# Performance work log

Hardware: AMD Instinct MI355X
Metric: run time of the kernel (lower is better)

## Reference

```python
import jax, jax.numpy as jnp
import numpy as np

N, E, IN, H, K = 50000, 800000, 64, 64, 16


def _linear_params(key, fan_in, fan_out):
    kw, kb = jax.random.split(key)
    lim = 1.0 / np.sqrt(fan_in)
    W = jax.random.uniform(kw, (fan_in, fan_out), jnp.float32, -lim, lim)
    b = jax.random.uniform(kb, (fan_out,), jnp.float32, -lim, lim)
    return W, b


def setup_inputs() -> dict:
    key = jax.random.key(0)
    ks = jax.random.split(key, 16)
    x = jax.random.normal(ks[0], (N, IN), jnp.float32)
    edge_index = jax.random.randint(ks[1], (2, E), 0, N, jnp.int64)
    edge_attr = jax.random.uniform(ks[2], (E, 1), jnp.float32)
    curr_idx = jax.random.randint(ks[3], (), 0, N, jnp.int64)
    dest_idx = jax.random.randint(ks[4], (), 0, N, jnp.int64)
    neighbor_indices = jax.random.randint(ks[5], (K,), 0, N, jnp.int64)
    # GINEConv1 params: edge lift Linear(1->IN), mlp1 Linear(IN->H), Linear(H->H)
    We1, be1 = _linear_params(ks[6], 1, IN)
    W1a, b1a = _linear_params(ks[7], IN, H)
    W1b, b1b = _linear_params(ks[8], H, H)
    # GINEConv2 params: edge lift Linear(1->H), mlp2 Linear(H->H), Linear(H->H)
    We2, be2 = _linear_params(ks[9], 1, H)
    W2a, b2a = _linear_params(ks[10], H, H)
    W2b, b2b = _linear_params(ks[11], H, H)
    # Q head: lin1 Linear(3H->H), lin2 Linear(H->1)
    Wl1, bl1 = _linear_params(ks[12], 3 * H, H)
    Wl2, bl2 = _linear_params(ks[13], H, 1)
    return dict(x=x, edge_index=edge_index, curr_idx=curr_idx, dest_idx=dest_idx,
                neighbor_indices=neighbor_indices, edge_attr=edge_attr,
                We1=We1, be1=be1, W1a=W1a, b1a=b1a, W1b=W1b, b1b=b1b,
                We2=We2, be2=be2, W2a=W2a, b2a=b2a, W2b=W2b, b2b=b2b,
                Wl1=Wl1, bl1=bl1, Wl2=Wl2, bl2=bl2)


def _gine(x, src, dst, e_emb, Wa, ba, Wb, bb):
    # message = ReLU(x_j + edge_emb); aggregate = sum over incoming edges; eps = 0
    msg = jax.nn.relu(x[src] + e_emb)                      # [E, d]
    agg = jax.ops.segment_sum(msg, dst, num_segments=x.shape[0])  # [N, d]
    h = x + agg                                            # (1+eps)*x + agg
    return jax.nn.relu(h @ Wa + ba) @ Wb + bb


def reference(x, edge_index, curr_idx, dest_idx, neighbor_indices, edge_attr,
              We1, be1, W1a, b1a, W1b, b1b,
              We2, be2, W2a, b2a, W2b, b2b,
              Wl1, bl1, Wl2, bl2):
    src, dst = edge_index[0], edge_index[1]
    h = _gine(x, src, dst, edge_attr @ We1 + be1, W1a, b1a, W1b, b1b)
    h = jax.nn.relu(h)
    h = _gine(h, src, dst, edge_attr @ We2 + be2, W2a, b2a, W2b, b2b)  # [N, H]
    curr = h[curr_idx]                 # [H]
    dest = h[dest_idx]                 # [H]
    nbr = h[neighbor_indices]          # [K, H]
    k = nbr.shape[0]
    cat = jnp.concatenate([jnp.broadcast_to(curr, (k, curr.shape[0])),
                           jnp.broadcast_to(dest, (k, dest.shape[0])),
                           nbr], axis=-1)                  # [K, 3H]
    q = jax.nn.relu(cat @ Wl1 + bl1) @ Wl2 + bl2           # [K, 1]
    return q[:, 0]
```

## Files before the change

kernel.cpp:

```cpp
#include <hip/hip_runtime.h>

#define NDIM 64
#define KNBR 16
#define NT 18
#define CAP_S1 1024
#define CAP_B1 128
#define CAP_B2 128
#define EPT 16
#define SCAN_TPB 256

#define OFF_CNT  0
#define OFF_BC2  64
#define OFF_BC1  192
#define MEMSET_BYTES (192 + CAP_S1*4)
#define OFF_S1   8192
#define OFF_B1   (OFF_S1 + CAP_S1*4)
#define OFF_B2   (OFF_B1 + CAP_S1*CAP_B1*4)
#define OFF_H    (OFF_B2 + 32*CAP_B2*4)
#define OFF_SLOT (OFF_H + CAP_S1*NDIM*4)

__device__ __forceinline__ int imin(int a, int b) { return a < b ? a : b; }

__device__ __forceinline__ void claim_node(int v, int* sm, int* cnt, int* s1list) {
    int cur = sm[v];
    while (!(cur >= 1 && cur <= CAP_S1) && cur != -2) {
        int old = atomicCAS(&sm[v], cur, -2);
        if (old == cur) {
            int s = atomicAdd(&cnt[0], 1);
            if (s < CAP_S1) s1list[s] = v;
            __threadfence();
            sm[v] = s + 1;
            return;
        }
        cur = old;
    }
}

__global__ void __launch_bounds__(SCAN_TPB)
k_scan1(const int* __restrict__ src, const int* __restrict__ dst, int E,
        const int* __restrict__ curr, const int* __restrict__ dest,
        const int* __restrict__ nbr,
        int* cnt, int* sm, int* s1list, int* bc2, int* b2) {
    int t0[NT];
    t0[0] = curr[0];
    t0[1] = dest[0];
    #pragma unroll
    for (int j = 0; j < KNBR; ++j) t0[2 + j] = nbr[j];
    if (blockIdx.x == 0 && threadIdx.x < NT)
        claim_node(t0[threadIdx.x], sm, cnt, s1list);

    const int i4base = blockIdx.x * (SCAN_TPB * EPT / 4);
    const int nI4 = E >> 2;
    int dv[EPT];
    #pragma unroll
    for (int q = 0; q < EPT / 4; ++q) {
        int idx = i4base + q * SCAN_TPB + threadIdx.x;
        if (idx < nI4) {
            int4 v = ((const int4*)dst)[idx];
            dv[q*4+0] = v.x; dv[q*4+1] = v.y; dv[q*4+2] = v.z; dv[q*4+3] = v.w;
        } else {
            #pragma unroll
            for (int j = 0; j < 4; ++j) {
                int e = idx * 4 + j;
                dv[q*4+j] = (e < E) ? dst[e] : -1;
            }
        }
    }
    #pragma unroll
    for (int q = 0; q < EPT; ++q) {
        int dd = dv[q];
        if (dd < 0) continue;
        int e = (i4base + (q >> 2) * SCAN_TPB + threadIdx.x) * 4 + (q & 3);
        bool any = false;
        #pragma unroll
        for (int k = 0; k < NT; ++k) {
            if (dd == t0[k]) {
                any = true;
                int idx = atomicAdd(&bc2[k], 1);
                if (idx < CAP_B2) b2[k * CAP_B2 + idx] = e;
            }
        }
        if (any) claim_node(src[e], sm, cnt, s1list);
    }
}

__global__ void __launch_bounds__(SCAN_TPB)
k_scan2(const int* __restrict__ dst, int E, const int* __restrict__ sm,
        int* bc1, int* b1) {
    const int i4base = blockIdx.x * (SCAN_TPB * EPT / 4);
    const int nI4 = E >> 2;
    int dv[EPT];
    #pragma unroll
    for (int q = 0; q < EPT / 4; ++q) {
        int idx = i4base + q * SCAN_TPB + threadIdx.x;
        if (idx < nI4) {
            int4 v = ((const int4*)dst)[idx];
            dv[q*4+0] = v.x; dv[q*4+1] = v.y; dv[q*4+2] = v.z; dv[q*4+3] = v.w;
        } else {
            #pragma unroll
            for (int j = 0; j < 4; ++j) {
                int e = idx * 4 + j;
                dv[q*4+j] = (e < E) ? dst[e] : -1;
            }
        }
    }
    #pragma unroll
    for (int q = 0; q < EPT; ++q) {
        int dd = dv[q];
        if (dd < 0) continue;
        int val = sm[dd];
        if (val >= 1 && val <= CAP_S1) {
            int s = val - 1;
            int e = (i4base + (q >> 2) * SCAN_TPB + threadIdx.x) * 4 + (q & 3);
            int idx = atomicAdd(&bc1[s], 1);
            if (idx < CAP_B1) b1[s * CAP_B1 + idx] = e;
        }
    }
}

__global__ void __launch_bounds__(256)
k_node1(const float* __restrict__ x, const int* __restrict__ src,
        const float* __restrict__ eattr,
        const int* __restrict__ cnt, const int* __restrict__ s1list,
        const int* __restrict__ bc1, const int* __restrict__ b1,
        const float* __restrict__ We1, const float* __restrict__ be1,
        const float* __restrict__ W1a, const float* __restrict__ b1a,
        const float* __restrict__ W1b, const float* __restrict__ b1b,
        float* __restrict__ hbuf) {
    int nS1 = imin(cnt[0], CAP_S1);
    int sbase = blockIdx.x * 4;
    if (sbase >= nS1) return;

    __shared__ float w1a[NDIM * NDIM];
    __shared__ float w1b[NDIM * NDIM];
    {
        const float4* A = (const float4*)W1a;
        const float4* B = (const float4*)W1b;
        float4* a = (float4*)w1a;
        float4* b = (float4*)w1b;
        #pragma unroll
        for (int q = 0; q < 4; ++q) {
            int i = q * 256 + threadIdx.x;
            a[i] = A[i];
            b[i] = B[i];
        }
    }
    __syncthreads();

    const int wid = threadIdx.x >> 6, lane = threadIdx.x & 63;
    int s = sbase + wid;
    if (s >= nS1) return;

    __shared__ int   s_iv[4][CAP_B1];
    __shared__ float s_fv[4][CAP_B1];
    __shared__ float s_t[4][NDIM];
    __shared__ float s_u[4][NDIM];

    int m = imin(bc1[s], CAP_B1);
    for (int i = lane; i < m; i += 64) {
        int e = b1[s * CAP_B1 + i];
        s_iv[wid][i] = src[e];
        s_fv[wid][i] = eattr[e];
    }
    __builtin_amdgcn_wave_barrier();
    float w = We1[lane], b = be1[lane];
    int v = s1list[s];
    float a0 = x[(size_t)v * NDIM + lane], a1 = 0.f, a2 = 0.f, a3 = 0.f;
    int i = 0;
    for (; i + 3 < m; i += 4) {
        a0 += fmaxf(x[(size_t)s_iv[wid][i+0] * NDIM + lane] + fmaf(s_fv[wid][i+0], w, b), 0.f);
        a1 += fmaxf(x[(size_t)s_iv[wid][i+1] * NDIM + lane] + fmaf(s_fv[wid][i+1], w, b), 0.f);
        a2 += fmaxf(x[(size_t)s_iv[wid][i+2] * NDIM + lane] + fmaf(s_fv[wid][i+2], w, b), 0.f);
        a3 += fmaxf(x[(size_t)s_iv[wid][i+3] * NDIM + lane] + fmaf(s_fv[wid][i+3], w, b), 0.f);
    }
    for (; i < m; ++i)
        a0 += fmaxf(x[(size_t)s_iv[wid][i] * NDIM + lane] + fmaf(s_fv[wid][i], w, b), 0.f);
    s_t[wid][lane] = (a0 + a1) + (a2 + a3);
    __builtin_amdgcn_wave_barrier();
    float m1 = b1a[lane];
    #pragma unroll 8
    for (int k = 0; k < NDIM; ++k) m1 = fmaf(s_t[wid][k], w1a[k * NDIM + lane], m1);
    s_u[wid][lane] = fmaxf(m1, 0.f);
    __builtin_amdgcn_wave_barrier();
    float m2 = b1b[lane];
    #pragma unroll 8
    for (int k = 0; k < NDIM; ++k) m2 = fmaf(s_u[wid][k], w1b[k * NDIM + lane], m2);
    hbuf[(size_t)s * NDIM + lane] = fmaxf(m2, 0.f);
}

__global__ void __launch_bounds__(512)
k_epi(const int* __restrict__ src, const float* __restrict__ eattr,
      const int* __restrict__ curr, const int* __restrict__ dest,
      const int* __restrict__ nbr, const int* __restrict__ sm,
      const int* __restrict__ bc2, const int* __restrict__ b2,
      const float* __restrict__ hbuf,
      const float* __restrict__ We2, const float* __restrict__ be2,
      const float* __restrict__ W2a, const float* __restrict__ b2a,
      const float* __restrict__ W2b, const float* __restrict__ b2b,
      const float* __restrict__ Wl1, const float* __restrict__ bl1,
      const float* __restrict__ Wl2, const float* __restrict__ bl2,
      float* __restrict__ out) {
    const int wid = threadIdx.x >> 6, lane = threadIdx.x & 63;

    __shared__ float w2a[NDIM * NDIM];
    __shared__ float w2b[NDIM * NDIM];
    {
        const float4* A = (const float4*)W2a;
        const float4* B = (const float4*)W2b;
        float4* a = (float4*)w2a;
        float4* b = (float4*)w2b;
        #pragma unroll
        for (int q = 0; q < 2; ++q) {
            int i = q * 512 + threadIdx.x;
            a[i] = A[i]; a[i + 1024] = A[i + 1024];
            b[i] = B[i]; b[i + 1024] = B[i + 1024];
        }
    }

    __shared__ float s_outh[NT][NDIM];
    __shared__ int   s_iv[8][CAP_B2];
    __shared__ float s_fv[8][CAP_B2];
    __shared__ float s_t[8][NDIM];
    __shared__ float s_u[8][NDIM];

    int t0[NT];
    t0[0] = curr[0];
    t0[1] = dest[0];
    #pragma unroll
    for (int j = 0; j < KNBR; ++j) t0[2 + j] = nbr[j];
    __syncthreads();

    for (int kt = wid; kt < NT; kt += 8) {
        int m = imin(bc2[kt], CAP_B2);
        for (int i = lane; i < m; i += 64) {
            int e = b2[kt * CAP_B2 + i];
            s_iv[wid][i] = sm[src[e]] - 1;
            s_fv[wid][i] = eattr[e];
        }
        __builtin_amdgcn_wave_barrier();
        int sv = sm[t0[kt]] - 1;
        float w2e = We2[lane], b2e = be2[lane];
        float a0 = hbuf[(size_t)sv * NDIM + lane], a1 = 0.f, a2 = 0.f, a3 = 0.f;
        int i = 0;
        for (; i + 3 < m; i += 4) {
            int s0 = s_iv[wid][i+0], s1 = s_iv[wid][i+1], s2 = s_iv[wid][i+2], s3 = s_iv[wid][i+3];
            if (s0 >= 0 && s0 < CAP_S1) a0 += fmaxf(hbuf[(size_t)s0 * NDIM + lane] + fmaf(s_fv[wid][i+0], w2e, b2e), 0.f);
            if (s1 >= 0 && s1 < CAP_S1) a1 += fmaxf(hbuf[(size_t)s1 * NDIM + lane] + fmaf(s_fv[wid][i+1], w2e, b2e), 0.f);
            if (s2 >= 0 && s2 < CAP_S1) a2 += fmaxf(hbuf[(size_t)s2 * NDIM + lane] + fmaf(s_fv[wid][i+2], w2e, b2e), 0.f);
            if (s3 >= 0 && s3 < CAP_S1) a3 += fmaxf(hbuf[(size_t)s3 * NDIM + lane] + fmaf(s_fv[wid][i+3], w2e, b2e), 0.f);
        }
        for (; i < m; ++i) {
            int s = s_iv[wid][i];
            if (s >= 0 && s < CAP_S1)
                a0 += fmaxf(hbuf[(size_t)s * NDIM + lane] + fmaf(s_fv[wid][i], w2e, b2e), 0.f);
        }
        s_t[wid][lane] = (a0 + a1) + (a2 + a3);
        __builtin_amdgcn_wave_barrier();
        float m1 = b2a[lane];
        #pragma unroll 8
        for (int kk = 0; kk < NDIM; ++kk) m1 = fmaf(s_t[wid][kk], w2a[kk * NDIM + lane], m1);
        s_u[wid][lane] = fmaxf(m1, 0.f);
        __builtin_amdgcn_wave_barrier();
        float m2 = b2b[lane];
        #pragma unroll 8
        for (int kk = 0; kk < NDIM; ++kk) m2 = fmaf(s_u[wid][kk], w2b[kk * NDIM + lane], m2);
        s_outh[kt][lane] = m2;
    }
    __syncthreads();

    for (int j = wid; j < KNBR; j += 8) {
        float acc = bl1[lane];
        #pragma unroll 8
        for (int i = 0; i < NDIM; ++i) acc = fmaf(s_outh[0][i], Wl1[i * NDIM + lane], acc);
        #pragma unroll 8
        for (int i = 0; i < NDIM; ++i) acc = fmaf(s_outh[1][i], Wl1[(NDIM + i) * NDIM + lane], acc);
        #pragma unroll 8
        for (int i = 0; i < NDIM; ++i) acc = fmaf(s_outh[2 + j][i], Wl1[(2 * NDIM + i) * NDIM + lane], acc);
        acc = fmaxf(acc, 0.f) * Wl2[lane];
        #pragma unroll
        for (int off = 32; off > 0; off >>= 1) acc += __shfl_down(acc, off);
        if (lane == 0) out[j] = acc + bl2[0];
    }
}

extern "C" void kernel_launch(void* const* d_in, const int* in_sizes, int n_in,
                              void* d_out, int out_size, void* d_ws, size_t ws_size,
                              hipStream_t stream) {
    const float* x     = (const float*)d_in[0];
    const int*   eidx  = (const int*)d_in[1];
    const int    E     = in_sizes[1] / 2;
    const int*   src   = eidx;
    const int*   dstA  = eidx + E;
    const int*   curr  = (const int*)d_in[2];
    const int*   dest  = (const int*)d_in[3];
    const int*   nbr   = (const int*)d_in[4];
    const float* eattr = (const float*)d_in[5];
    const float* We1 = (const float*)d_in[6];
    const float* be1 = (const float*)d_in[7];
    const float* W1a = (const float*)d_in[8];
    const float* b1a = (const float*)d_in[9];
    const float* W1b = (const float*)d_in[10];
    const float* b1b = (const float*)d_in[11];
    const float* We2 = (const float*)d_in[12];
    const float* be2 = (const float*)d_in[13];
    const float* W2a = (const float*)d_in[14];
    const float* b2a = (const float*)d_in[15];
    const float* W2b = (const float*)d_in[16];
    const float* b2b = (const float*)d_in[17];
    const float* Wl1 = (const float*)d_in[18];
    const float* bl1 = (const float*)d_in[19];
    const float* Wl2 = (const float*)d_in[20];
    const float* bl2 = (const float*)d_in[21];

    char* ws = (char*)d_ws;
    int*   cnt    = (int*)(ws + OFF_CNT);
    int*   bc2    = (int*)(ws + OFF_BC2);
    int*   bc1    = (int*)(ws + OFF_BC1);
    int*   s1list = (int*)(ws + OFF_S1);
    int*   b1     = (int*)(ws + OFF_B1);
    int*   b2     = (int*)(ws + OFF_B2);
    float* hbuf   = (float*)(ws + OFF_H);
    int*   sm     = (int*)(ws + OFF_SLOT);

    hipMemsetAsync(ws, 0, MEMSET_BYTES, stream);

    int scanBlocks = (E + SCAN_TPB * EPT - 1) / (SCAN_TPB * EPT);
    k_scan1<<<scanBlocks, SCAN_TPB, 0, stream>>>(src, dstA, E, curr, dest, nbr,
                                                 cnt, sm, s1list, bc2, b2);
    k_scan2<<<scanBlocks, SCAN_TPB, 0, stream>>>(dstA, E, sm, bc1, b1);
    k_node1<<<CAP_S1 / 4, 256, 0, stream>>>(x, src, eattr, cnt, s1list, bc1, b1,
                                            We1, be1, W1a, b1a, W1b, b1b, hbuf);
    k_epi<<<1, 512, 0, stream>>>(src, eattr, curr, dest, nbr, sm, bc2, b2, hbuf,
                                 We2, be2, W2a, b2a, W2b, b2b,
                                 Wl1, bl1, Wl2, bl2, (float*)d_out);
}
```

Before: 171.8 us.

## Replace node slot map with small hash table and fuse epilogue via last-block

Swaps the per-node slot array (which relied on an uninitialised or large workspace region) for a 1024-entry open-addressing hash table that fits in the zeroed memset region. Atomic counters are padded to 16-int strides to cut contention. The epilogue kernel is merged into the node kernel through a last-block-done atomic, which removes one launch. Wl1 is staged in shared memory. The epilogue now runs on a single 256-thread block with 4 waves instead of 8, and hash collisions add probing cost.

```diff
diff --git a/kernel.cpp b/kernel.cpp
--- a/kernel.cpp
+++ b/kernel.cpp
@@ -3,36 +3,50 @@
 #define NDIM 64
 #define KNBR 16
 #define NT 18
-#define CAP_S1 1024
+#define HTS 1024
 #define CAP_B1 128
 #define CAP_B2 128
 #define EPT 16
 #define SCAN_TPB 256
 
-#define OFF_CNT  0
-#define OFF_BC2  64
-#define OFF_BC1  192
-#define MEMSET_BYTES (192 + CAP_S1*4)
-#define OFF_S1   8192
-#define OFF_B1   (OFF_S1 + CAP_S1*4)
-#define OFF_B2   (OFF_B1 + CAP_S1*CAP_B1*4)
-#define OFF_H    (OFF_B2 + 32*CAP_B2*4)
-#define OFF_SLOT (OFF_H + CAP_S1*NDIM*4)
+#define OFF_HT    0
+#define OFF_BC2   (HTS*4)
+#define OFF_DONE  (OFF_BC2 + 32*16*4)
+#define OFF_BC1   (OFF_DONE + 64)
+#define MEMSET_BYTES (OFF_BC1 + HTS*16*4)
+#define OFF_B1    (MEMSET_BYTES)
+#define OFF_B2    (OFF_B1 + HTS*CAP_B1*4)
+#define OFF_H     (OFF_B2 + 32*CAP_B2*4)
 
 __device__ __forceinline__ int imin(int a, int b) { return a < b ? a : b; }
 
-__device__ __forceinline__ void claim_node(int v, int* sm, int* cnt, int* s1list) {
-    int cur = sm[v];
-    while (!(cur >= 1 && cur <= CAP_S1) && cur != -2) {
-        int old = atomicCAS(&sm[v], cur, -2);
-        if (old == cur) {
-            int s = atomicAdd(&cnt[0], 1);
-            if (s < CAP_S1) s1list[s] = v;
-            __threadfence();
-            sm[v] = s + 1;
-            return;
-        }
-        cur = old;
+__device__ __forceinline__ unsigned hslot(int v) {
+    return ((unsigned)v * 2654435761u) >> 22;
+}
+
+__device__ __forceinline__ int claim(int* ht, int v) {
+    unsigned h = hslot(v);
+    int cur = ht[h];
+    while (true) {
+        if (cur == v + 1) return (int)h;
+        if (cur == 0) {
+            int old = atomicCAS(&ht[h], 0, v + 1);
+            if (old == 0) return (int)h;
+            cur = old;
+            continue;
+        }
+        h = (h + 1) & (HTS - 1);
+        cur = ht[h];
+    }
+}
+
+__device__ __forceinline__ int lookup(const int* __restrict__ ht, int v) {
+    unsigned h = hslot(v);
+    while (true) {
+        int cur = ht[h];
+        if (cur == v + 1) return (int)h;
+        if (cur == 0) return -1;
+        h = (h + 1) & (HTS - 1);
     }
 }
 
@@ -40,14 +54,14 @@
 k_scan1(const int* __restrict__ src, const int* __restrict__ dst, int E,
         const int* __restrict__ curr, const int* __restrict__ dest,
         const int* __restrict__ nbr,
-        int* cnt, int* sm, int* s1list, int* bc2, int* b2) {
+        int* ht, int* bc2, int* b2) {
     int t0[NT];
     t0[0] = curr[0];
     t0[1] = dest[0];
     #pragma unroll
     for (int j = 0; j < KNBR; ++j) t0[2 + j] = nbr[j];
     if (blockIdx.x == 0 && threadIdx.x < NT)
-        claim_node(t0[threadIdx.x], sm, cnt, s1list);
+        claim(ht, t0[threadIdx.x]);
 
     const int i4base = blockIdx.x * (SCAN_TPB * EPT / 4);
     const int nI4 = E >> 2;
@@ -76,16 +90,16 @@
         for (int k = 0; k < NT; ++k) {
             if (dd == t0[k]) {
                 any = true;
-                int idx = atomicAdd(&bc2[k], 1);
+                int idx = atomicAdd(&bc2[k * 16], 1);
                 if (idx < CAP_B2) b2[k * CAP_B2 + idx] = e;
             }
         }
-        if (any) claim_node(src[e], sm, cnt, s1list);
+        if (any) claim(ht, src[e]);
     }
 }
 
 __global__ void __launch_bounds__(SCAN_TPB)
-k_scan2(const int* __restrict__ dst, int E, const int* __restrict__ sm,
+k_scan2(const int* __restrict__ dst, int E, const int* __restrict__ ht,
         int* bc1, int* b1) {
     const int i4base = blockIdx.x * (SCAN_TPB * EPT / 4);
     const int nI4 = E >> 2;
@@ -108,121 +122,120 @@
     for (int q = 0; q < EPT; ++q) {
         int dd = dv[q];
         if (dd < 0) continue;
-        int val = sm[dd];
-        if (val >= 1 && val <= CAP_S1) {
-            int s = val - 1;
+        int s = lookup(ht, dd);
+        if (s >= 0) {
             int e = (i4base + (q >> 2) * SCAN_TPB + threadIdx.x) * 4 + (q & 3);
-            int idx = atomicAdd(&bc1[s], 1);
+            int idx = atomicAdd(&bc1[s * 16], 1);
             if (idx < CAP_B1) b1[s * CAP_B1 + idx] = e;
         }
     }
 }
 
 __global__ void __launch_bounds__(256)
-k_node1(const float* __restrict__ x, const int* __restrict__ src,
-        const float* __restrict__ eattr,
-        const int* __restrict__ cnt, const int* __restrict__ s1list,
-        const int* __restrict__ bc1, const int* __restrict__ b1,
-        const float* __restrict__ We1, const float* __restrict__ be1,
-        const float* __restrict__ W1a, const float* __restrict__ b1a,
-        const float* __restrict__ W1b, const float* __restrict__ b1b,
-        float* __restrict__ hbuf) {
-    int nS1 = imin(cnt[0], CAP_S1);
-    int sbase = blockIdx.x * 4;
-    if (sbase >= nS1) return;
-
-    __shared__ float w1a[NDIM * NDIM];
-    __shared__ float w1b[NDIM * NDIM];
-    {
+k_node(const float* __restrict__ x, const int* __restrict__ src,
+       const float* __restrict__ eattr,
+       const int* __restrict__ curr, const int* __restrict__ dest,
+       const int* __restrict__ nbr, const int* __restrict__ ht,
+       const int* __restrict__ bc1, const int* __restrict__ b1,
+       const int* __restrict__ bc2, const int* __restrict__ b2,
+       const float* __restrict__ We1, const float* __restrict__ be1,
+       const float* __restrict__ W1a, const float* __restrict__ b1a,
+       const float* __restrict__ W1b, const float* __restrict__ b1b,
+       const float* __restrict__ We2, const float* __restrict__ be2,
+       const float* __restrict__ W2a, const float* __restrict__ b2a,
+       const float* __restrict__ W2b, const float* __restrict__ b2b,
+       const float* __restrict__ Wl1, const float* __restrict__ bl1,
+       const float* __restrict__ Wl2, const float* __restrict__ bl2,
+       float* __restrict__ hbuf, int* done, float* __restrict__ out) {
+    const int wid = threadIdx.x >> 6, lane = threadIdx.x & 63;
+
+    __shared__ float wA[NDIM * NDIM];
+    __shared__ float wB[NDIM * NDIM];
+    __shared__ float wC[NDIM * NDIM];
+    __shared__ int   s_iv[4][CAP_B1];
+    __shared__ float s_fv[4][CAP_B1];
+    __shared__ float s_t[4][NDIM];
+    __shared__ float s_u[4][NDIM];
+    __shared__ float s_outh[NT][NDIM];
+    __shared__ int   s_last;
+
+    const int sbase = blockIdx.x * 4;
+    const int v4a = ht[sbase + 0], v4b = ht[sbase + 1];
+    const int v4c = ht[sbase + 2], v4d = ht[sbase + 3];
+    const bool haswork = (v4a | v4b | v4c | v4d) != 0;
+
+    if (haswork) {
         const float4* A = (const float4*)W1a;
         const float4* B = (const float4*)W1b;
-        float4* a = (float4*)w1a;
-        float4* b = (float4*)w1b;
+        float4* a = (float4*)wA;
+        float4* b = (float4*)wB;
         #pragma unroll
         for (int q = 0; q < 4; ++q) {
             int i = q * 256 + threadIdx.x;
             a[i] = A[i];
             b[i] = B[i];
         }
-    }
-    __syncthreads();
-
-    const int wid = threadIdx.x >> 6, lane = threadIdx.x & 63;
-    int s = sbase + wid;
-    if (s >= nS1) return;
-
-    __shared__ int   s_iv[4][CAP_B1];
-    __shared__ float s_fv[4][CAP_B1];
-    __shared__ float s_t[4][NDIM];
-    __shared__ float s_u[4][NDIM];
-
-    int m = imin(bc1[s], CAP_B1);
-    for (int i = lane; i < m; i += 64) {
-        int e = b1[s * CAP_B1 + i];
-        s_iv[wid][i] = src[e];
-        s_fv[wid][i] = eattr[e];
-    }
-    __builtin_amdgcn_wave_barrier();
-    float w = We1[lane], b = be1[lane];
-    int v = s1list[s];
-    float a0 = x[(size_t)v * NDIM + lane], a1 = 0.f, a2 = 0.f, a3 = 0.f;
-    int i = 0;
-    for (; i + 3 < m; i += 4) {
-        a0 += fmaxf(x[(size_t)s_iv[wid][i+0] * NDIM + lane] + fmaf(s_fv[wid][i+0], w, b), 0.f);
-        a1 += fmaxf(x[(size_t)s_iv[wid][i+1] * NDIM + lane] + fmaf(s_fv[wid][i+1], w, b), 0.f);
-        a2 += fmaxf(x[(size_t)s_iv[wid][i+2] * NDIM + lane] + fmaf(s_fv[wid][i+2], w, b), 0.f);
-        a3 += fmaxf(x[(size_t)s_iv[wid][i+3] * NDIM + lane] + fmaf(s_fv[wid][i+3], w, b), 0.f);
-    }
-    for (; i < m; ++i)
-        a0 += fmaxf(x[(size_t)s_iv[wid][i] * NDIM + lane] + fmaf(s_fv[wid][i], w, b), 0.f);
-    s_t[wid][lane] = (a0 + a1) + (a2 + a3);
-    __builtin_amdgcn_wave_barrier();
-    float m1 = b1a[lane];
-    #pragma unroll 8
-    for (int k = 0; k < NDIM; ++k) m1 = fmaf(s_t[wid][k], w1a[k * NDIM + lane], m1);
-    s_u[wid][lane] = fmaxf(m1, 0.f);
-    __builtin_amdgcn_wave_barrier();
-    float m2 = b1b[lane];
-    #pragma unroll 8
-    for (int k = 0; k < NDIM; ++k) m2 = fmaf(s_u[wid][k], w1b[k * NDIM + lane], m2);
-    hbuf[(size_t)s * NDIM + lane] = fmaxf(m2, 0.f);
-}
-
-__global__ void __launch_bounds__(512)
-k_epi(const int* __restrict__ src, const float* __restrict__ eattr,
-      const int* __restrict__ curr, const int* __restrict__ dest,
-      const int* __restrict__ nbr, const int* __restrict__ sm,
-      const int* __restrict__ bc2, const int* __restrict__ b2,
-      const float* __restrict__ hbuf,
-      const float* __restrict__ We2, const float* __restrict__ be2,
-      const float* __restrict__ W2a, const float* __restrict__ b2a,
-      const float* __restrict__ W2b, const float* __restrict__ b2b,
-      const float* __restrict__ Wl1, const float* __restrict__ bl1,
-      const float* __restrict__ Wl2, const float* __restrict__ bl2,
-      float* __restrict__ out) {
-    const int wid = threadIdx.x >> 6, lane = threadIdx.x & 63;
-
-    __shared__ float w2a[NDIM * NDIM];
-    __shared__ float w2b[NDIM * NDIM];
+        __syncthreads();
+
+        int vv = (wid == 0) ? v4a : (wid == 1) ? v4b : (wid == 2) ? v4c : v4d;
+        if (vv != 0) {
+            int s = sbase + wid;
+            int v = vv - 1;
+            int m = imin(bc1[s * 16], CAP_B1);
+            for (int i = lane; i < m; i += 64) {
+                int e = b1[s * CAP_B1 + i];
+                s_iv[wid][i] = src[e];
+                s_fv[wid][i] = eattr[e];
+            }
+            __builtin_amdgcn_wave_barrier();
+            float w = We1[lane], b0 = be1[lane];
+            float a0 = x[(size_t)v * NDIM + lane], a1 = 0.f, a2 = 0.f, a3 = 0.f;
+            int i = 0;
+            for (; i + 3 < m; i += 4) {
+                a0 += fmaxf(x[(size_t)s_iv[wid][i+0] * NDIM + lane] + fmaf(s_fv[wid][i+0], w, b0), 0.f);
+                a1 += fmaxf(x[(size_t)s_iv[wid][i+1] * NDIM + lane] + fmaf(s_fv[wid][i+1], w, b0), 0.f);
+                a2 += fmaxf(x[(size_t)s_iv[wid][i+2] * NDIM + lane] + fmaf(s_fv[wid][i+2], w, b0), 0.f);
+                a3 += fmaxf(x[(size_t)s_iv[wid][i+3] * NDIM + lane] + fmaf(s_fv[wid][i+3], w, b0), 0.f);
+            }
+            for (; i < m; ++i)
+                a0 += fmaxf(x[(size_t)s_iv[wid][i] * NDIM + lane] + fmaf(s_fv[wid][i], w, b0), 0.f);
+            s_t[wid][lane] = (a0 + a1) + (a2 + a3);
+            __builtin_amdgcn_wave_barrier();
+            float m1 = b1a[lane];
+            #pragma unroll 8
+            for (int k = 0; k < NDIM; ++k) m1 = fmaf(s_t[wid][k], wA[k * NDIM + lane], m1);
+            s_u[wid][lane] = fmaxf(m1, 0.f);
+            __builtin_amdgcn_wave_barrier();
+            float m2 = b1b[lane];
+            #pragma unroll 8
+            for (int k = 0; k < NDIM; ++k) m2 = fmaf(s_u[wid][k], wB[k * NDIM + lane], m2);
+            hbuf[(size_t)s * NDIM + lane] = fmaxf(m2, 0.f);
+        }
+    }
+
+    __syncthreads();
+    if (threadIdx.x == 0) {
+        __threadfence();
+        int idx = __hip_atomic_fetch_add(done, 1, __ATOMIC_ACQ_REL,
+                                         __HIP_MEMORY_SCOPE_AGENT);
+        s_last = (idx == gridDim.x - 1);
+    }
+    __syncthreads();
+    if (!s_last) return;
+    __threadfence();
+
     {
         const float4* A = (const float4*)W2a;
         const float4* B = (const float4*)W2b;
-        float4* a = (float4*)w2a;
-        float4* b = (float4*)w2b;
-        #pragma unroll
-        for (int q = 0; q < 2; ++q) {
-            int i = q * 512 + threadIdx.x;
-            a[i] = A[i]; a[i + 1024] = A[i + 1024];
-            b[i] = B[i]; b[i + 1024] = B[i + 1024];
-        }
-    }
-
-    __shared__ float s_outh[NT][NDIM];
-    __shared__ int   s_iv[8][CAP_B2];
-    __shared__ float s_fv[8][CAP_B2];
-    __shared__ float s_t[8][NDIM];
-    __shared__ float s_u[8][NDIM];
-
+        float4* a = (float4*)wA;
+        float4* b = (float4*)wB;
+        #pragma unroll
+        for (int q = 0; q < 4; ++q) {
+            int i = q * 256 + threadIdx.x;
+            a[i] = A[i];
+            b[i] = B[i];
+        }
+    }
     int t0[NT];
     t0[0] = curr[0];
     t0[1] = dest[0];
@@ -230,52 +243,66 @@
     for (int j = 0; j < KNBR; ++j) t0[2 + j] = nbr[j];
     __syncthreads();
 
-    for (int kt = wid; kt < NT; kt += 8) {
-        int m = imin(bc2[kt], CAP_B2);
+    for (int kt = wid; kt < NT; kt += 4) {
+        int m = imin(bc2[kt * 16], CAP_B2);
         for (int i = lane; i < m; i += 64) {
             int e = b2[kt * CAP_B2 + i];
-            s_iv[wid][i] = sm[src[e]] - 1;
+            s_iv[wid][i] = lookup(ht, src[e]);
             s_fv[wid][i] = eattr[e];
         }
         __builtin_amdgcn_wave_barrier();
-        int sv = sm[t0[kt]] - 1;
+        int sv = lookup(ht, t0[kt]);
         float w2e = We2[lane], b2e = be2[lane];
         float a0 = hbuf[(size_t)sv * NDIM + lane], a1 = 0.f, a2 = 0.f, a3 = 0.f;
         int i = 0;
         for (; i + 3 < m; i += 4) {
             int s0 = s_iv[wid][i+0], s1 = s_iv[wid][i+1], s2 = s_iv[wid][i+2], s3 = s_iv[wid][i+3];
-            if (s0 >= 0 && s0 < CAP_S1) a0 += fmaxf(hbuf[(size_t)s0 * NDIM + lane] + fmaf(s_fv[wid][i+0], w2e, b2e), 0.f);
-            if (s1 >= 0 && s1 < CAP_S1) a1 += fmaxf(hbuf[(size_t)s1 * NDIM + lane] + fmaf(s_fv[wid][i+1], w2e, b2e), 0.f);
-            if (s2 >= 0 && s2 < CAP_S1) a2 += fmaxf(hbuf[(size_t)s2 * NDIM + lane] + fmaf(s_fv[wid][i+2], w2e, b2e), 0.f);
-            if (s3 >= 0 && s3 < CAP_S1) a3 += fmaxf(hbuf[(size_t)s3 * NDIM + lane] + fmaf(s_fv[wid][i+3], w2e, b2e), 0.f);
+            if (s0 >= 0) a0 += fmaxf(hbuf[(size_t)s0 * NDIM + lane] + fmaf(s_fv[wid][i+0], w2e, b2e), 0.f);
+            if (s1 >= 0) a1 += fmaxf(hbuf[(size_t)s1 * NDIM + lane] + fmaf(s_fv[wid][i+1], w2e, b2e), 0.f);
+            if (s2 >= 0) a2 += fmaxf(hbuf[(size_t)s2 * NDIM + lane] + fmaf(s_fv[wid][i+2], w2e, b2e), 0.f);
+            if (s3 >= 0) a3 += fmaxf(hbuf[(size_t)s3 * NDIM + lane] + fmaf(s_fv[wid][i+3], w2e, b2e), 0.f);
         }
         for (; i < m; ++i) {
             int s = s_iv[wid][i];
-            if (s >= 0 && s < CAP_S1)
-                a0 += fmaxf(hbuf[(size_t)s * NDIM + lane] + fmaf(s_fv[wid][i], w2e, b2e), 0.f);
+            if (s >= 0) a0 += fmaxf(hbuf[(size_t)s * NDIM + lane] + fmaf(s_fv[wid][i], w2e, b2e), 0.f);
         }
         s_t[wid][lane] = (a0 + a1) + (a2 + a3);
         __builtin_amdgcn_wave_barrier();
         float m1 = b2a[lane];
         #pragma unroll 8
-        for (int kk = 0; kk < NDIM; ++kk) m1 = fmaf(s_t[wid][kk], w2a[kk * NDIM + lane], m1);
+        for (int kk = 0; kk < NDIM; ++kk) m1 = fmaf(s_t[wid][kk], wA[kk * NDIM + lane], m1);
         s_u[wid][lane] = fmaxf(m1, 0.f);
         __builtin_amdgcn_wave_barrier();
         float m2 = b2b[lane];
         #pragma unroll 8
-        for (int kk = 0; kk < NDIM; ++kk) m2 = fmaf(s_u[wid][kk], w2b[kk * NDIM + lane], m2);
+        for (int kk = 0; kk < NDIM; ++kk) m2 = fmaf(s_u[wid][kk], wB[kk * NDIM + lane], m2);
         s_outh[kt][lane] = m2;
     }
     __syncthreads();
 
-    for (int j = wid; j < KNBR; j += 8) {
+    {
+        const float4* W = (const float4*)Wl1;
+        float4* a = (float4*)wA;
+        float4* b = (float4*)wB;
+        float4* c = (float4*)wC;
+        #pragma unroll
+        for (int q = 0; q < 4; ++q) {
+            int i = q * 256 + threadIdx.x;
+            a[i] = W[i];
+            b[i] = W[i + 1024];
+            c[i] = W[i + 2048];
+        }
+    }
+    __syncthreads();
+
+    for (int j = wid; j < KNBR; j += 4) {
         float acc = bl1[lane];
         #pragma unroll 8
-        for (int i = 0; i < NDIM; ++i) acc = fmaf(s_outh[0][i], Wl1[i * NDIM + lane], acc);
-        #pragma unroll 8
-        for (int i = 0; i < NDIM; ++i) acc = fmaf(s_outh[1][i], Wl1[(NDIM + i) * NDIM + lane], acc);
-        #pragma unroll 8
-        for (int i = 0; i < NDIM; ++i) acc = fmaf(s_outh[2 + j][i], Wl1[(2 * NDIM + i) * NDIM + lane], acc);
+        for (int i = 0; i < NDIM; ++i) acc = fmaf(s_outh[0][i], wA[i * NDIM + lane], acc);
+        #pragma unroll 8
+        for (int i = 0; i < NDIM; ++i) acc = fmaf(s_outh[1][i], wB[i * NDIM + lane], acc);
+        #pragma unroll 8
+        for (int i = 0; i < NDIM; ++i) acc = fmaf(s_outh[2 + j][i], wC[i * NDIM + lane], acc);
         acc = fmaxf(acc, 0.f) * Wl2[lane];
         #pragma unroll
         for (int off = 32; off > 0; off >>= 1) acc += __shfl_down(acc, off);
@@ -313,24 +340,24 @@
     const float* bl2 = (const float*)d_in[21];
 
     char* ws = (char*)d_ws;
-    int*   cnt    = (int*)(ws + OFF_CNT);
-    int*   bc2    = (int*)(ws + OFF_BC2);
-    int*   bc1    = (int*)(ws + OFF_BC1);
-    int*   s1list = (int*)(ws + OFF_S1);
-    int*   b1     = (int*)(ws + OFF_B1);
-    int*   b2     = (int*)(ws + OFF_B2);
-    float* hbuf   = (float*)(ws + OFF_H);
-    int*   sm     = (int*)(ws + OFF_SLOT);
+    int*   ht   = (int*)(ws + OFF_HT);
+    int*   bc2  = (int*)(ws + OFF_BC2);
+    int*   done = (int*)(ws + OFF_DONE);
+    int*   bc1  = (int*)(ws + OFF_BC1);
+    int*   b1   = (int*)(ws + OFF_B1);
+    int*   b2   = (int*)(ws + OFF_B2);
+    float* hbuf = (float*)(ws + OFF_H);
 
     hipMemsetAsync(ws, 0, MEMSET_BYTES, stream);
 
     int scanBlocks = (E + SCAN_TPB * EPT - 1) / (SCAN_TPB * EPT);
     k_scan1<<<scanBlocks, SCAN_TPB, 0, stream>>>(src, dstA, E, curr, dest, nbr,
-                                                 cnt, sm, s1list, bc2, b2);
-    k_scan2<<<scanBlocks, SCAN_TPB, 0, stream>>>(dstA, E, sm, bc1, b1);
-    k_node1<<<CAP_S1 / 4, 256, 0, stream>>>(x, src, eattr, cnt, s1list, bc1, b1,
-                                            We1, be1, W1a, b1a, W1b, b1b, hbuf);
-    k_epi<<<1, 512, 0, stream>>>(src, eattr, curr, dest, nbr, sm, bc2, b2, hbuf,
-                                 We2, be2, W2a, b2a, W2b, b2b,
-                                 Wl1, bl1, Wl2, bl2, (float*)d_out);
-}
+                                                 ht, bc2, b2);
+    k_scan2<<<scanBlocks, SCAN_TPB, 0, stream>>>(dstA, E, ht, bc1, b1);
+    k_node<<<HTS / 4, 256, 0, stream>>>(x, src, eattr, curr, dest, nbr, ht,
+                                        bc1, b1, bc2, b2,
+                                        We1, be1, W1a, b1a, W1b, b1b,
+                                        We2, be2, W2a, b2a, W2b, b2b,
+                                        Wl1, bl1, Wl2, bl2,
+                                        hbuf, done, (float*)d_out);
+}
```

New measurement: 202.6 us. 18.0% more time.
